# Kernel optimization log

Hardware: AMD Instinct MI355X
Metric: run time of the kernel (lower is better)

Reference implementation:

```python
import math
import jax, jax.numpy as jnp
import numpy as np

DRAGON_ITERATIONS = 12
DRAGON_SMOOTHING = 0.1


def _dragon_patterns(iterations=DRAGON_ITERATIONS, smoothing=DRAGON_SMOOTHING):
    """Deterministic (non-learned) Dragon curve patterns, matching torch impl."""
    patterns = [np.array([0.5], dtype=np.float32)]
    kernel = np.ones(3, dtype=np.float32) / 3.0
    for _ in range(1, iterations):
        prev = patterns[-1]
        n = len(prev)
        newp = np.zeros(2 * n + 1, dtype=np.float32)
        newp[:n] = prev
        newp[n] = 0.5
        newp[n + 1:] = 1.0 - prev[::-1]
        if smoothing > 0:
            # conv1d with kernel_size=3, padding=1 (zero pad) == np.convolve 'same'
            newp = np.convolve(newp, kernel, mode='same').astype(np.float32)
        newp = (newp - newp.min()) / (newp.max() - newp.min() + 1e-8)
        patterns.append(newp.astype(np.float32))
    return patterns

_PATTERNS = _dragon_patterns()


def _interp_pattern(seq_len):
    """Linearly interpolate selected dragon pattern to seq_len (static shapes)."""
    it = min(int(math.log2(seq_len)), DRAGON_ITERATIONS - 1)
    pattern = _PATTERNS[it]
    if len(pattern) == seq_len:
        w = pattern.copy()
    else:
        x_old = np.linspace(0.0, 1.0, len(pattern), dtype=np.float64)
        x_new = np.linspace(0.0, 1.0, seq_len, dtype=np.float64)
        w = np.interp(x_new, x_old, pattern.astype(np.float64)).astype(np.float32)
    return it, jnp.asarray(w)


def setup_inputs() -> dict:
    key = jax.random.key(0)
    ks = jax.random.split(key, 8)
    B, S, D = 8, 2048, 512
    query = jax.random.normal(ks[0], (B, S, D), dtype=jnp.float32)
    k = jax.random.normal(ks[1], (B, S, D), dtype=jnp.float32)
    value = jax.random.normal(ks[2], (B, S, D), dtype=jnp.float32)
    pattern_scale = jnp.ones((DRAGON_ITERATIONS,), dtype=jnp.float32)
    pattern_bias = jnp.zeros((DRAGON_ITERATIONS,), dtype=jnp.float32)
    w1 = jax.random.normal(ks[3], (DRAGON_ITERATIONS, 64), dtype=jnp.float32) * (1.0 / math.sqrt(DRAGON_ITERATIONS))
    b1 = jnp.zeros((64,), dtype=jnp.float32)
    w2 = jax.random.normal(ks[4], (64, 1), dtype=jnp.float32) * (1.0 / 8.0)
    b2 = jnp.zeros((1,), dtype=jnp.float32)
    return {"query": query, "key": k, "value": value,
            "pattern_scale": pattern_scale, "pattern_bias": pattern_bias,
            "w1": w1, "b1": b1, "w2": w2, "b2": b2}


def reference(query, key, value, pattern_scale, pattern_bias, w1, b1, w2, b2):
    B, S, D = key.shape
    it, base_w = _interp_pattern(S)
    # learned affine + softplus on dragon weights
    dragon_w = jax.nn.softplus(base_w * pattern_scale[it] + pattern_bias[it])  # [S]
    weighted_keys = key * dragon_w[None, :, None]                              # [B,S,D]
    scores = jnp.einsum('bqd,bkd->bqk', query, weighted_keys) / math.sqrt(D)   # [B,S,S]
    attn = jax.nn.softmax(scores, axis=-1)
    # blend factor from one-hot iteration features through tiny MLP
    feat = jax.nn.one_hot(it, DRAGON_ITERATIONS, dtype=query.dtype)            # [12]
    h = jax.nn.relu(feat @ w1 + b1)
    blend = jax.nn.sigmoid(h @ w2 + b2)                                        # [1]
    blend = blend[0]
    final_attn = blend * attn + (1.0 - blend) / S                              # uniform blend
    out = jnp.einsum('bqk,bkd->bqd', final_attn, value)                        # [B,S,D]
    # original does output.squeeze(1); S>1 so it's a no-op here
    return out
```

## Files before the change

### kernel.cpp

```cpp
#include <hip/hip_runtime.h>
#include <cstdint>

#define DEV __device__ __forceinline__

typedef float f32x4 __attribute__((ext_vector_type(4)));
typedef short s16x8 __attribute__((ext_vector_type(8)));

DEV unsigned short f2bf(float f){
    unsigned u = __builtin_bit_cast(unsigned, f);
    u = u + 0x7fffu + ((u >> 16) & 1u);
    return (unsigned short)(u >> 16);
}
DEV float bf2f(unsigned short h){
    unsigned u = ((unsigned)h) << 16;
    return __builtin_bit_cast(float, u);
}

typedef const void __attribute__((address_space(1)))* gcp;
typedef void __attribute__((address_space(3)))* lp;
DEV void gload_lds16(const void* g, void* l){
    __builtin_amdgcn_global_load_lds((gcp)g, (lp)l, 16, 0, 0);
}

__global__ __launch_bounds__(256) void k_stage1(
    const float* __restrict__ Q, const float* __restrict__ V,
    const float* __restrict__ scale, const float* __restrict__ bias,
    const float* __restrict__ w1, const float* __restrict__ b1,
    const float* __restrict__ w2, const float* __restrict__ b2,
    float* __restrict__ dragon_w, float* __restrict__ blend_out,
    unsigned short* __restrict__ Qb, unsigned short* __restrict__ Vt,
    float* __restrict__ vmean_part)
{
    __shared__ float sh[8704];
    int tid = threadIdx.x;
    int bx  = blockIdx.x;

    if (bx == 0){
        float* A    = sh;
        float* Bb   = sh + 4096;
        float* sred = sh + 8192;
        if (tid == 0) A[0] = 0.5f;
        __syncthreads();
        int len = 1;
        for (int it = 1; it < 12; ++it){
            int n = len, nl = 2*n + 1;
            for (int i = tid; i < nl; i += 256){
                float v;
                if (i < n)       v = A[i];
                else if (i == n) v = 0.5f;
                else             v = 1.0f - A[2*n - i];
                Bb[i] = v;
            }
            __syncthreads();
            const float third = 1.0f/3.0f;
            for (int i = tid; i < nl; i += 256){
                float s = Bb[i]*third;
                if (i > 0)    s += Bb[i-1]*third;
                if (i < nl-1) s += Bb[i+1]*third;
                A[i] = s;
            }
            __syncthreads();
            float mn = 3.4e38f, mx = -3.4e38f;
            for (int i = tid; i < nl; i += 256){ float v = A[i]; mn = fminf(mn,v); mx = fmaxf(mx,v); }
            sred[tid] = mn; sred[256 + tid] = mx;
            __syncthreads();
            for (int off = 128; off > 0; off >>= 1){
                if (tid < off){
                    sred[tid]       = fminf(sred[tid],       sred[tid+off]);
                    sred[256 + tid] = fmaxf(sred[256 + tid], sred[256 + tid + off]);
                }
                __syncthreads();
            }
            float lo = sred[0], den = sred[256] - lo + 1e-8f;
            for (int i = tid; i < nl; i += 256) A[i] = (A[i] - lo) / den;
            len = nl;
            __syncthreads();
        }
        float sc = scale[11], bi = bias[11];
        for (int i = tid; i < 2048; i += 256){
            float x = A[2*i]*sc + bi;
            dragon_w[i] = fmaxf(x, 0.f) + log1pf(__expf(-fabsf(x)));
        }
        if (tid < 64){
            float h = fmaxf(w1[11*64 + tid] + b1[tid], 0.f);
            float c = h * w2[tid];
            for (int off = 32; off > 0; off >>= 1) c += __shfl_xor(c, off, 64);
            if (tid == 0) blend_out[0] = 1.f/(1.f + __expf(-(c + b2[0])));
        }
        return;
    }

    if (bx <= 2048){
        const long long total4 = (long long)8*2048*512/4;
        long long stride = 2048LL*256;
        for (long long i = (long long)(bx-1)*256 + tid; i < total4; i += stride){
            long long base = i*4;
            const float4 q = *(const float4*)(Q + base);
            ushort4 qo;
            qo.x = f2bf(q.x); qo.y = f2bf(q.y); qo.z = f2bf(q.z); qo.w = f2bf(q.w);
            *(ushort4*)(Qb + base) = qo;
        }
        return;
    }

    int t = bx - 2049;
    int stile = t & 31, dtile = (t >> 5) & 7, b = t >> 8;
    int s0 = stile*64, d0 = dtile*64;
    float (*tile)[66] = (float(*)[66])sh;
    float* red = sh + 4352;
    int tx = tid & 63, ty = tid >> 6;
    const float* src = V + ((long long)b*2048 + s0)*512 + d0;
    #pragma unroll
    for (int r = 0; r < 16; ++r){
        int row = r*4 + ty;
        tile[row][tx] = src[(long long)row*512 + tx];
    }
    __syncthreads();
    unsigned short* dst = Vt + ((long long)b*512 + d0)*2048 + s0;
    #pragma unroll
    for (int r = 0; r < 16; ++r){
        int drow = r*4 + ty;
        dst[(long long)drow*2048 + tx] = f2bf(tile[tx][drow]);
    }
    int dcol = tid & 63, sp = tid >> 6;
    float s = 0.f;
    #pragma unroll
    for (int ii = 0; ii < 16; ++ii) s += tile[sp*16 + ii][dcol];
    red[sp*64 + dcol] = s;
    __syncthreads();
    if (sp == 0){
        float tot = red[dcol] + red[64+dcol] + red[128+dcol] + red[192+dcol];
        vmean_part[stile*4096 + b*512 + d0 + dcol] = tot * (1.0f/2048.0f);
    }
}

__global__ __launch_bounds__(256) void k_stage2(
    const float* __restrict__ K, const float* __restrict__ dragon_w,
    const float* __restrict__ vmean_part,
    unsigned short* __restrict__ Kb, float* __restrict__ vmean)
{
    int bx = blockIdx.x, tid = threadIdx.x;
    if (bx < 16){
        int idx = bx*256 + tid;
        float s = 0.f;
        #pragma unroll
        for (int st = 0; st < 32; ++st) s += vmean_part[st*4096 + idx];
        vmean[idx] = s;
        return;
    }
    const long long total4 = (long long)8*2048*512/4;
    long long stride = 2048LL*256;
    for (long long i = (long long)(bx-16)*256 + tid; i < total4; i += stride){
        long long base = i*4;
        int s = (int)((base >> 9) & 2047);
        float w = dragon_w[s];
        const float4 k = *(const float4*)(K + base);
        ushort4 ko;
        ko.x = f2bf(k.x*w); ko.y = f2bf(k.y*w); ko.z = f2bf(k.z*w); ko.w = f2bf(k.w*w);
        *(ushort4*)(Kb + base) = ko;
    }
}

#define SCALE_QK 0.04419417382415922f

__global__ __launch_bounds__(256) void k_gemm_qk(
    const unsigned short* __restrict__ Qb, const unsigned short* __restrict__ Kb,
    unsigned short* __restrict__ Sp)
{
    __shared__ unsigned short At[128*64];
    __shared__ unsigned short Bt[128*64];
    int tid = threadIdx.x;
    int lane = tid & 63, wave = tid >> 6;
    int wm = wave >> 1, wn = wave & 1;
    int ln = lane & 15, q4 = lane >> 4;
    int sx = ln & 7;
    int q0 = blockIdx.y*128, k0 = blockIdx.x*128, b = blockIdx.z;
    const unsigned short* Abase = Qb + ((long long)b*2048 + q0)*512;
    const unsigned short* Bbase = Kb + ((long long)b*2048 + k0)*512;

    f32x4 acc[4][4];
    #pragma unroll
    for (int i = 0; i < 4; ++i)
        #pragma unroll
        for (int j = 0; j < 4; ++j) acc[i][j] = (f32x4)0.0f;

    int cc = lane & 7;
    int rg = lane >> 3;
    for (int kt = 0; kt < 8; ++kt){
        #pragma unroll
        for (int c = 0; c < 4; ++c){
            int chunk = wave*4 + c;
            int row = chunk*8 + rg;
            int gc  = cc ^ (row & 7);
            gload_lds16(Abase + (long long)row*512 + kt*64 + gc*8, &At[chunk*512]);
            gload_lds16(Bbase + (long long)row*512 + kt*64 + gc*8, &Bt[chunk*512]);
        }
        __syncthreads();
        #pragma unroll
        for (int ks = 0; ks < 2; ++ks){
            s16x8 af[4], bfr[4];
            int cs = ((ks*4 + q4) ^ sx) * 8;
            #pragma unroll
            for (int i = 0; i < 4; ++i)
                af[i] = *(const s16x8*)&At[(wm*64 + i*16 + ln)*64 + cs];
            #pragma unroll
            for (int j = 0; j < 4; ++j)
                bfr[j] = *(const s16x8*)&Bt[(wn*64 + j*16 + ln)*64 + cs];
            #pragma unroll
            for (int i = 0; i < 4; ++i)
                #pragma unroll
                for (int j = 0; j < 4; ++j)
                    acc[i][j] = __builtin_amdgcn_mfma_f32_16x16x32_bf16(af[i], bfr[j], acc[i][j], 0, 0, 0);
        }
        __syncthreads();
    }
    unsigned short* outp = Sp + (long long)b*2048*2048;
    #pragma unroll
    for (int i = 0; i < 4; ++i){
        #pragma unroll
        for (int j = 0; j < 4; ++j){
            #pragma unroll
            for (int r = 0; r < 4; ++r){
                int q = q0 + wm*64 + i*16 + q4*4 + r;
                int k = k0 + wn*64 + j*16 + ln;
                float v = __expf(acc[i][j][r] * SCALE_QK);
                outp[(long long)q*2048 + k] = f2bf(v);
            }
        }
    }
}

__global__ __launch_bounds__(256) void k_gemm_pv(
    const unsigned short* __restrict__ Sp, const unsigned short* __restrict__ Vt,
    const float* __restrict__ vmean, const float* __restrict__ blendp,
    float* __restrict__ out)
{
    __shared__ unsigned short At[128*64];
    __shared__ unsigned short Bt[128*64];
    __shared__ float l_sh[128];
    int tid = threadIdx.x;
    int lane = tid & 63, wave = tid >> 6;
    int wm = wave >> 1, wn = wave & 1;
    int ln = lane & 15, q4 = lane >> 4;
    int sx = ln & 7;
    int q0 = blockIdx.y*128, d0 = blockIdx.x*128, b = blockIdx.z;
    const unsigned short* Abase = Sp + (long long)b*2048*2048 + (long long)q0*2048;
    const unsigned short* Bbase = Vt + ((long long)b*512 + d0)*2048;

    f32x4 acc[4][4];
    #pragma unroll
    for (int i = 0; i < 4; ++i)
        #pragma unroll
        for (int j = 0; j < 4; ++j) acc[i][j] = (f32x4)0.0f;
    float lsum[4] = {0.f, 0.f, 0.f, 0.f};

    int cc = lane & 7;
    int rg = lane >> 3;
    for (int kt = 0; kt < 32; ++kt){
        #pragma unroll
        for (int c = 0; c < 4; ++c){
            int chunk = wave*4 + c;
            int row = chunk*8 + rg;
            int gc  = cc ^ (row & 7);
            gload_lds16(Abase + (long long)row*2048 + kt*64 + gc*8, &At[chunk*512]);
            gload_lds16(Bbase + (long long)row*2048 + kt*64 + gc*8, &Bt[chunk*512]);
        }
        __syncthreads();
        #pragma unroll
        for (int ks = 0; ks < 2; ++ks){
            s16x8 af[4], bfr[4];
            int cs = ((ks*4 + q4) ^ sx) * 8;
            #pragma unroll
            for (int i = 0; i < 4; ++i)
                af[i] = *(const s16x8*)&At[(wm*64 + i*16 + ln)*64 + cs];
            #pragma unroll
            for (int j = 0; j < 4; ++j)
                bfr[j] = *(const s16x8*)&Bt[(wn*64 + j*16 + ln)*64 + cs];
            if (wn == 0){
                #pragma unroll
                for (int i = 0; i < 4; ++i){
                    float s = 0.f;
                    #pragma unroll
                    for (int jj = 0; jj < 8; ++jj) s += bf2f((unsigned short)af[i][jj]);
                    lsum[i] += s;
                }
            }
            #pragma unroll
            for (int i = 0; i < 4; ++i)
                #pragma unroll
                for (int j = 0; j < 4; ++j)
                    acc[i][j] = __builtin_amdgcn_mfma_f32_16x16x32_bf16(af[i], bfr[j], acc[i][j], 0, 0, 0);
        }
        __syncthreads();
    }
    if (wn == 0){
        #pragma unroll
        for (int i = 0; i < 4; ++i){
            float v = lsum[i];
            v += __shfl_xor(v, 16, 64);
            v += __shfl_xor(v, 32, 64);
            if (lane < 16) l_sh[wm*64 + i*16 + lane] = v;
        }
    }
    __syncthreads();

    float blend = blendp[0];
    float ib = 1.0f - blend;
    float* obase = out + ((long long)b*2048 + q0)*512 + d0;
    float vm[4];
    #pragma unroll
    for (int j = 0; j < 4; ++j) vm[j] = vmean[b*512 + d0 + wn*64 + j*16 + ln];
    #pragma unroll
    for (int i = 0; i < 4; ++i){
        #pragma unroll
        for (int r = 0; r < 4; ++r){
            int ql = wm*64 + i*16 + q4*4 + r;
            float linv = 1.0f / l_sh[ql];
            #pragma unroll
            for (int j = 0; j < 4; ++j){
                int dl = wn*64 + j*16 + ln;
                obase[(long long)ql*512 + dl] = blend*acc[i][j][r]*linv + ib*vm[j];
            }
        }
    }
}

extern "C" void kernel_launch(void* const* d_in, const int* in_sizes, int n_in,
                              void* d_out, int out_size, void* d_ws, size_t ws_size,
                              hipStream_t stream)
{
    (void)in_sizes; (void)n_in; (void)out_size; (void)ws_size;
    const float* Q  = (const float*)d_in[0];
    const float* K  = (const float*)d_in[1];
    const float* V  = (const float*)d_in[2];
    const float* ps = (const float*)d_in[3];
    const float* pb = (const float*)d_in[4];
    const float* w1 = (const float*)d_in[5];
    const float* b1 = (const float*)d_in[6];
    const float* w2 = (const float*)d_in[7];
    const float* b2 = (const float*)d_in[8];
    float* out = (float*)d_out;

    char* ws = (char*)d_ws;
    float* dragon_w        = (float*)(ws);
    float* blend           = (float*)(ws + 8192);
    float* vmean           = (float*)(ws + 16384);
    float* vmean_part      = (float*)(ws + 32768);
    size_t off = 32768 + (size_t)512*1024;
    unsigned short* Qb     = (unsigned short*)(ws + off);
    unsigned short* Kb     = (unsigned short*)(ws + off + (size_t)16*1024*1024);
    unsigned short* Vt     = (unsigned short*)(ws + off + (size_t)32*1024*1024);
    unsigned short* Sp     = (unsigned short*)(ws + off + (size_t)48*1024*1024);

    hipLaunchKernelGGL(k_stage1,  dim3(4097),      dim3(256), 0, stream,
                       Q, V, ps, pb, w1, b1, w2, b2, dragon_w, blend, Qb, Vt, vmean_part);
    hipLaunchKernelGGL(k_stage2,  dim3(2064),      dim3(256), 0, stream,
                       K, dragon_w, vmean_part, Kb, vmean);
    hipLaunchKernelGGL(k_gemm_qk, dim3(16, 16, 8), dim3(256), 0, stream,
                       Qb, Kb, Sp);
    hipLaunchKernelGGL(k_gemm_pv, dim3(4, 16, 8),  dim3(256), 0, stream,
                       Sp, Vt, vmean, blend, out);
}
```

Baseline: 253.2 us.

## Rewrite QK and PV GEMMs with 256-row tiles, multi-stage LDS pipelining, fused row sums

Both GEMM kernels move to 512-thread blocks with 256-row tiles and a four-slot LDS ring. Global-to-LDS loads for the next k-steps are interleaved with MFMA phases using explicit barriers, vmcnt waits and setprio. The softmax row sums are now computed in the QK epilogue from the rounded bf16 exp values and written as per-block partials, which the PV kernel reduces. This removes the per-iteration sum work from the PV inner loop. In exchange, the hand-written barrier and waitcnt scheduling is fragile, and the larger tiles reduce the grid size and may raise register pressure.

```diff
diff --git a/kernel.cpp b/kernel.cpp
--- a/kernel.cpp
+++ b/kernel.cpp
@@ -21,6 +21,11 @@
 DEV void gload_lds16(const void* g, void* l){
     __builtin_amdgcn_global_load_lds((gcp)g, (lp)l, 16, 0, 0);
 }
+
+DEV void bar(){ asm volatile("s_barrier" ::: "memory"); }
+DEV void lgkm0(){ asm volatile("s_waitcnt lgkmcnt(0)" ::: "memory"); }
+#define WAIT_VM(n) asm volatile("s_waitcnt vmcnt(" #n ")" ::: "memory")
+#define MFMA16(a,b,c) __builtin_amdgcn_mfma_f32_16x16x32_bf16(a,b,c,0,0,0)
 
 __global__ __launch_bounds__(256) void k_stage1(
     const float* __restrict__ Q, const float* __restrict__ V,
@@ -163,163 +168,276 @@
 
 #define SCALE_QK 0.04419417382415922f
 
-__global__ __launch_bounds__(256) void k_gemm_qk(
+__global__ __launch_bounds__(512, 2) void k_gemm_qk(
     const unsigned short* __restrict__ Qb, const unsigned short* __restrict__ Kb,
-    unsigned short* __restrict__ Sp)
+    unsigned short* __restrict__ Sp, float* __restrict__ lpart)
 {
-    __shared__ unsigned short At[128*64];
-    __shared__ unsigned short Bt[128*64];
-    int tid = threadIdx.x;
-    int lane = tid & 63, wave = tid >> 6;
-    int wm = wave >> 1, wn = wave & 1;
-    int ln = lane & 15, q4 = lane >> 4;
-    int sx = ln & 7;
-    int q0 = blockIdx.y*128, k0 = blockIdx.x*128, b = blockIdx.z;
-    const unsigned short* Abase = Qb + ((long long)b*2048 + q0)*512;
-    const unsigned short* Bbase = Kb + ((long long)b*2048 + k0)*512;
+    __shared__ unsigned short At[4*8192];
+    __shared__ unsigned short Bt[4*8192];
+    const int tid  = threadIdx.x;
+    const int lane = tid & 63, wave = tid >> 6;
+    const int wm = wave >> 2, wn = wave & 3;
+    const int ln = lane & 15, q4 = lane >> 4;
+    const int q0 = blockIdx.y*256, k0 = blockIdx.x*256, b = blockIdx.z;
+    const unsigned short* Ab = Qb + ((long long)b*2048 + q0)*512;
+    const unsigned short* Bb = Kb + ((long long)b*2048 + k0)*512;
+    const int cc = lane & 7, rg = lane >> 3;
+    const int gcx = cc ^ rg;
+    const int ch0 = wave*2, ch1 = wave*2 + 1;
+
+    f32x4 acc[8][4];
+    #pragma unroll
+    for (int m = 0; m < 8; ++m)
+        #pragma unroll
+        for (int n = 0; n < 4; ++n) acc[m][n] = (f32x4)0.f;
+
+    s16x8 af[8], b0[4], b1[4];
+
+    auto STA = [&](int kt, int h){
+        unsigned short* d = &At[(((kt<<1) + h) & 3) * 8192];
+        const unsigned short* s = Ab + (long long)(h*128)*512 + kt*64 + gcx*8;
+        gload_lds16(s + (long long)(ch0*8 + rg)*512, d + ch0*512);
+        gload_lds16(s + (long long)(ch1*8 + rg)*512, d + ch1*512);
+    };
+    auto STB = [&](int kt, int h){
+        unsigned short* d = &Bt[(((kt<<1) + h) & 3) * 8192];
+        const unsigned short* s = Bb + (long long)(h*128)*512 + kt*64 + gcx*8;
+        gload_lds16(s + (long long)(ch0*8 + rg)*512, d + ch0*512);
+        gload_lds16(s + (long long)(ch1*8 + rg)*512, d + ch1*512);
+    };
+    auto LDA = [&](int t, int ks){
+        const unsigned short* base = &At[(((t<<1) + wm) & 3) * 8192];
+        const int ccs = ((ks*4 + q4) ^ (ln & 7)) * 8;
+        #pragma unroll
+        for (int m = 0; m < 8; ++m)
+            af[m] = *(const s16x8*)&base[(m*16 + ln)*64 + ccs];
+    };
+    auto LDB = [&](int t, int ks, s16x8* bv){
+        const unsigned short* base = &Bt[(((t<<1) + (wn>>1)) & 3) * 8192];
+        const int ccs = ((ks*4 + q4) ^ (ln & 7)) * 8;
+        #pragma unroll
+        for (int n = 0; n < 4; ++n)
+            bv[n] = *(const s16x8*)&base[((wn&1)*64 + n*16 + ln)*64 + ccs];
+    };
+
+    STB(0,0); STB(0,1); STA(0,0); STA(0,1); STB(1,0); STB(1,1);
+    WAIT_VM(4);
+    bar();
+
+    for (int t = 0; t < 8; ++t){
+        const int t1 = (t+1) & 7, t2 = (t+2) & 7;
+        LDA(t, 0); LDB(t, 0, b0);
+        STA(t1, 0);
+        bar(); lgkm0();
+        __builtin_amdgcn_s_setprio(1);
+        #pragma unroll
+        for (int m = 0; m < 8; ++m){
+            acc[m][0] = MFMA16(af[m], b0[0], acc[m][0]);
+            acc[m][1] = MFMA16(af[m], b0[1], acc[m][1]);
+        }
+        __builtin_amdgcn_s_setprio(0);
+        bar();
+        LDB(t, 1, b1);
+        STA(t1, 1);
+        bar(); lgkm0();
+        __builtin_amdgcn_s_setprio(1);
+        #pragma unroll
+        for (int m = 0; m < 8; ++m){
+            acc[m][2] = MFMA16(af[m], b0[2], acc[m][2]);
+            acc[m][3] = MFMA16(af[m], b0[3], acc[m][3]);
+        }
+        __builtin_amdgcn_s_setprio(0);
+        bar();
+        LDA(t, 1);
+        STB(t2, 0);
+        bar(); lgkm0();
+        __builtin_amdgcn_s_setprio(1);
+        #pragma unroll
+        for (int m = 0; m < 8; ++m){
+            acc[m][0] = MFMA16(af[m], b1[0], acc[m][0]);
+            acc[m][1] = MFMA16(af[m], b1[1], acc[m][1]);
+        }
+        __builtin_amdgcn_s_setprio(0);
+        bar();
+        STB(t2, 1);
+        WAIT_VM(4);
+        bar();
+        __builtin_amdgcn_s_setprio(1);
+        #pragma unroll
+        for (int m = 0; m < 8; ++m){
+            acc[m][2] = MFMA16(af[m], b1[2], acc[m][2]);
+            acc[m][3] = MFMA16(af[m], b1[3], acc[m][3]);
+        }
+        __builtin_amdgcn_s_setprio(0);
+        bar();
+    }
+    WAIT_VM(0);
+    bar();
+
+    float* lred = (float*)At;
+    unsigned short* outp = Sp + (long long)b*2048*2048 + (long long)q0*2048 + k0;
+    #pragma unroll
+    for (int m = 0; m < 8; ++m){
+        float rs[4] = {0.f, 0.f, 0.f, 0.f};
+        #pragma unroll
+        for (int r = 0; r < 4; ++r){
+            int qrow = wm*128 + m*16 + q4*4 + r;
+            #pragma unroll
+            for (int n = 0; n < 4; ++n){
+                int kcol = wn*64 + n*16 + ln;
+                float v = __expf(acc[m][n][r] * SCALE_QK);
+                unsigned short h = f2bf(v);
+                outp[(long long)qrow*2048 + kcol] = h;
+                rs[r] += bf2f(h);
+            }
+        }
+        #pragma unroll
+        for (int r = 0; r < 4; ++r){
+            float v = rs[r];
+            v += __shfl_xor(v, 1, 16);
+            v += __shfl_xor(v, 2, 16);
+            v += __shfl_xor(v, 4, 16);
+            v += __shfl_xor(v, 8, 16);
+            if (ln == 0) lred[(wm*128 + m*16 + q4*4 + r)*4 + wn] = v;
+        }
+    }
+    bar();
+    if (tid < 256){
+        float lpv = lred[tid*4+0] + lred[tid*4+1] + lred[tid*4+2] + lred[tid*4+3];
+        lpart[((long long)b*8 + blockIdx.x)*2048 + q0 + tid] = lpv;
+    }
+}
+
+__global__ __launch_bounds__(512, 2) void k_gemm_pv(
+    const unsigned short* __restrict__ Sp, const unsigned short* __restrict__ Vt,
+    const float* __restrict__ lpart, const float* __restrict__ vmean,
+    const float* __restrict__ blendp, float* __restrict__ out)
+{
+    __shared__ unsigned short At[4*8192];
+    __shared__ unsigned short Bt[4*4096];
+    const int tid  = threadIdx.x;
+    const int lane = tid & 63, wave = tid >> 6;
+    const int wm = wave & 3, wn = wave >> 2;
+    const int ln = lane & 15, q4 = lane >> 4;
+    const int q0 = blockIdx.y*256, d0 = blockIdx.x*128, b = blockIdx.z;
+    const unsigned short* Ab = Sp + (long long)b*2048*2048 + (long long)q0*2048;
+    const unsigned short* Bb = Vt + ((long long)b*512 + d0)*2048;
+    const int cc = lane & 7, rg = lane >> 3;
+    const int gcx = cc ^ rg;
+    const int ch0 = wave*2, ch1 = wave*2 + 1;
 
     f32x4 acc[4][4];
     #pragma unroll
-    for (int i = 0; i < 4; ++i)
-        #pragma unroll
-        for (int j = 0; j < 4; ++j) acc[i][j] = (f32x4)0.0f;
-
-    int cc = lane & 7;
-    int rg = lane >> 3;
-    for (int kt = 0; kt < 8; ++kt){
-        #pragma unroll
-        for (int c = 0; c < 4; ++c){
-            int chunk = wave*4 + c;
-            int row = chunk*8 + rg;
-            int gc  = cc ^ (row & 7);
-            gload_lds16(Abase + (long long)row*512 + kt*64 + gc*8, &At[chunk*512]);
-            gload_lds16(Bbase + (long long)row*512 + kt*64 + gc*8, &Bt[chunk*512]);
-        }
-        __syncthreads();
-        #pragma unroll
-        for (int ks = 0; ks < 2; ++ks){
-            s16x8 af[4], bfr[4];
-            int cs = ((ks*4 + q4) ^ sx) * 8;
-            #pragma unroll
-            for (int i = 0; i < 4; ++i)
-                af[i] = *(const s16x8*)&At[(wm*64 + i*16 + ln)*64 + cs];
-            #pragma unroll
-            for (int j = 0; j < 4; ++j)
-                bfr[j] = *(const s16x8*)&Bt[(wn*64 + j*16 + ln)*64 + cs];
-            #pragma unroll
-            for (int i = 0; i < 4; ++i)
-                #pragma unroll
-                for (int j = 0; j < 4; ++j)
-                    acc[i][j] = __builtin_amdgcn_mfma_f32_16x16x32_bf16(af[i], bfr[j], acc[i][j], 0, 0, 0);
-        }
-        __syncthreads();
-    }
-    unsigned short* outp = Sp + (long long)b*2048*2048;
-    #pragma unroll
-    for (int i = 0; i < 4; ++i){
-        #pragma unroll
-        for (int j = 0; j < 4; ++j){
-            #pragma unroll
-            for (int r = 0; r < 4; ++r){
-                int q = q0 + wm*64 + i*16 + q4*4 + r;
-                int k = k0 + wn*64 + j*16 + ln;
-                float v = __expf(acc[i][j][r] * SCALE_QK);
-                outp[(long long)q*2048 + k] = f2bf(v);
-            }
-        }
-    }
-}
-
-__global__ __launch_bounds__(256) void k_gemm_pv(
-    const unsigned short* __restrict__ Sp, const unsigned short* __restrict__ Vt,
-    const float* __restrict__ vmean, const float* __restrict__ blendp,
-    float* __restrict__ out)
-{
-    __shared__ unsigned short At[128*64];
-    __shared__ unsigned short Bt[128*64];
-    __shared__ float l_sh[128];
-    int tid = threadIdx.x;
-    int lane = tid & 63, wave = tid >> 6;
-    int wm = wave >> 1, wn = wave & 1;
-    int ln = lane & 15, q4 = lane >> 4;
-    int sx = ln & 7;
-    int q0 = blockIdx.y*128, d0 = blockIdx.x*128, b = blockIdx.z;
-    const unsigned short* Abase = Sp + (long long)b*2048*2048 + (long long)q0*2048;
-    const unsigned short* Bbase = Vt + ((long long)b*512 + d0)*2048;
-
-    f32x4 acc[4][4];
-    #pragma unroll
-    for (int i = 0; i < 4; ++i)
-        #pragma unroll
-        for (int j = 0; j < 4; ++j) acc[i][j] = (f32x4)0.0f;
-    float lsum[4] = {0.f, 0.f, 0.f, 0.f};
-
-    int cc = lane & 7;
-    int rg = lane >> 3;
-    for (int kt = 0; kt < 32; ++kt){
-        #pragma unroll
-        for (int c = 0; c < 4; ++c){
-            int chunk = wave*4 + c;
-            int row = chunk*8 + rg;
-            int gc  = cc ^ (row & 7);
-            gload_lds16(Abase + (long long)row*2048 + kt*64 + gc*8, &At[chunk*512]);
-            gload_lds16(Bbase + (long long)row*2048 + kt*64 + gc*8, &Bt[chunk*512]);
-        }
-        __syncthreads();
-        #pragma unroll
-        for (int ks = 0; ks < 2; ++ks){
-            s16x8 af[4], bfr[4];
-            int cs = ((ks*4 + q4) ^ sx) * 8;
-            #pragma unroll
-            for (int i = 0; i < 4; ++i)
-                af[i] = *(const s16x8*)&At[(wm*64 + i*16 + ln)*64 + cs];
-            #pragma unroll
-            for (int j = 0; j < 4; ++j)
-                bfr[j] = *(const s16x8*)&Bt[(wn*64 + j*16 + ln)*64 + cs];
-            if (wn == 0){
-                #pragma unroll
-                for (int i = 0; i < 4; ++i){
-                    float s = 0.f;
-                    #pragma unroll
-                    for (int jj = 0; jj < 8; ++jj) s += bf2f((unsigned short)af[i][jj]);
-                    lsum[i] += s;
-                }
-            }
-            #pragma unroll
-            for (int i = 0; i < 4; ++i)
-                #pragma unroll
-                for (int j = 0; j < 4; ++j)
-                    acc[i][j] = __builtin_amdgcn_mfma_f32_16x16x32_bf16(af[i], bfr[j], acc[i][j], 0, 0, 0);
-        }
-        __syncthreads();
-    }
-    if (wn == 0){
-        #pragma unroll
-        for (int i = 0; i < 4; ++i){
-            float v = lsum[i];
-            v += __shfl_xor(v, 16, 64);
-            v += __shfl_xor(v, 32, 64);
-            if (lane < 16) l_sh[wm*64 + i*16 + lane] = v;
-        }
-    }
-    __syncthreads();
+    for (int m = 0; m < 4; ++m)
+        #pragma unroll
+        for (int n = 0; n < 4; ++n) acc[m][n] = (f32x4)0.f;
+
+    s16x8 af[4], b0[4], b1[4];
+
+    auto STA = [&](int kt, int h){
+        unsigned short* d = &At[(((kt<<1) + h) & 3) * 8192];
+        const unsigned short* s = Ab + (long long)(h*128)*2048 + kt*64 + gcx*8;
+        gload_lds16(s + (long long)(ch0*8 + rg)*2048, d + ch0*512);
+        gload_lds16(s + (long long)(ch1*8 + rg)*2048, d + ch1*512);
+    };
+    auto STB = [&](int kt, int h){
+        unsigned short* d = &Bt[(((kt<<1) + h) & 3) * 4096];
+        const unsigned short* s = Bb + (long long)(h*64 + wave*8 + rg)*2048 + kt*64 + gcx*8;
+        gload_lds16(s, d + wave*512);
+    };
+    auto LDA = [&](int t, int ks){
+        const unsigned short* base = &At[(((t<<1) + (wm>>1)) & 3) * 8192];
+        const int ccs = ((ks*4 + q4) ^ (ln & 7)) * 8;
+        #pragma unroll
+        for (int m = 0; m < 4; ++m)
+            af[m] = *(const s16x8*)&base[((wm&1)*64 + m*16 + ln)*64 + ccs];
+    };
+    auto LDB = [&](int t, int ks, s16x8* bv){
+        const unsigned short* base = &Bt[(((t<<1) + wn) & 3) * 4096];
+        const int ccs = ((ks*4 + q4) ^ (ln & 7)) * 8;
+        #pragma unroll
+        for (int n = 0; n < 4; ++n)
+            bv[n] = *(const s16x8*)&base[(n*16 + ln)*64 + ccs];
+    };
+
+    STB(0,0); STB(0,1); STA(0,0); STA(0,1); STB(1,0); STB(1,1);
+    WAIT_VM(2);
+    bar();
+
+    for (int t = 0; t < 32; ++t){
+        const int t1 = (t+1) & 31, t2 = (t+2) & 31;
+        LDA(t, 0); LDB(t, 0, b0);
+        STA(t1, 0);
+        bar(); lgkm0();
+        __builtin_amdgcn_s_setprio(1);
+        #pragma unroll
+        for (int m = 0; m < 4; ++m){
+            acc[m][0] = MFMA16(af[m], b0[0], acc[m][0]);
+            acc[m][1] = MFMA16(af[m], b0[1], acc[m][1]);
+        }
+        __builtin_amdgcn_s_setprio(0);
+        bar();
+        STA(t1, 1);
+        bar();
+        __builtin_amdgcn_s_setprio(1);
+        #pragma unroll
+        for (int m = 0; m < 4; ++m){
+            acc[m][2] = MFMA16(af[m], b0[2], acc[m][2]);
+            acc[m][3] = MFMA16(af[m], b0[3], acc[m][3]);
+        }
+        __builtin_amdgcn_s_setprio(0);
+        bar();
+        LDA(t, 1); LDB(t, 1, b1);
+        bar(); lgkm0();
+        __builtin_amdgcn_s_setprio(1);
+        #pragma unroll
+        for (int m = 0; m < 4; ++m){
+            acc[m][0] = MFMA16(af[m], b1[0], acc[m][0]);
+            acc[m][1] = MFMA16(af[m], b1[1], acc[m][1]);
+        }
+        __builtin_amdgcn_s_setprio(0);
+        bar();
+        STB(t2, 0); STB(t2, 1);
+        WAIT_VM(2);
+        bar();
+        __builtin_amdgcn_s_setprio(1);
+        #pragma unroll
+        for (int m = 0; m < 4; ++m){
+            acc[m][2] = MFMA16(af[m], b1[2], acc[m][2]);
+            acc[m][3] = MFMA16(af[m], b1[3], acc[m][3]);
+        }
+        __builtin_amdgcn_s_setprio(0);
+        bar();
+    }
+    WAIT_VM(0);
+    bar();
+
+    float* l_sh = (float*)Bt;
+    if (tid < 256){
+        float s = 0.f;
+        #pragma unroll
+        for (int kb = 0; kb < 8; ++kb)
+            s += lpart[((long long)b*8 + kb)*2048 + q0 + tid];
+        l_sh[tid] = 1.0f / s;
+    }
+    bar();
 
     float blend = blendp[0];
     float ib = 1.0f - blend;
     float* obase = out + ((long long)b*2048 + q0)*512 + d0;
     float vm[4];
     #pragma unroll
-    for (int j = 0; j < 4; ++j) vm[j] = vmean[b*512 + d0 + wn*64 + j*16 + ln];
-    #pragma unroll
-    for (int i = 0; i < 4; ++i){
+    for (int n = 0; n < 4; ++n) vm[n] = vmean[b*512 + d0 + wn*64 + n*16 + ln];
+    #pragma unroll
+    for (int m = 0; m < 4; ++m){
         #pragma unroll
         for (int r = 0; r < 4; ++r){
-            int ql = wm*64 + i*16 + q4*4 + r;
-            float linv = 1.0f / l_sh[ql];
+            int ql = wm*64 + m*16 + q4*4 + r;
+            float linv = l_sh[ql];
             #pragma unroll
-            for (int j = 0; j < 4; ++j){
-                int dl = wn*64 + j*16 + ln;
-                obase[(long long)ql*512 + dl] = blend*acc[i][j][r]*linv + ib*vm[j];
+            for (int n = 0; n < 4; ++n){
+                int dl = wn*64 + n*16 + ln;
+                obase[(long long)ql*512 + dl] = blend*acc[m][n][r]*linv + ib*vm[n];
             }
         }
     }
@@ -351,13 +469,14 @@
     unsigned short* Kb     = (unsigned short*)(ws + off + (size_t)16*1024*1024);
     unsigned short* Vt     = (unsigned short*)(ws + off + (size_t)32*1024*1024);
     unsigned short* Sp     = (unsigned short*)(ws + off + (size_t)48*1024*1024);
-
-    hipLaunchKernelGGL(k_stage1,  dim3(4097),      dim3(256), 0, stream,
+    float* lpart           = vmean_part;
+
+    hipLaunchKernelGGL(k_stage1,  dim3(4097),     dim3(256), 0, stream,
                        Q, V, ps, pb, w1, b1, w2, b2, dragon_w, blend, Qb, Vt, vmean_part);
-    hipLaunchKernelGGL(k_stage2,  dim3(2064),      dim3(256), 0, stream,
+    hipLaunchKernelGGL(k_stage2,  dim3(2064),     dim3(256), 0, stream,
                        K, dragon_w, vmean_part, Kb, vmean);
-    hipLaunchKernelGGL(k_gemm_qk, dim3(16, 16, 8), dim3(256), 0, stream,
-                       Qb, Kb, Sp);
-    hipLaunchKernelGGL(k_gemm_pv, dim3(4, 16, 8),  dim3(256), 0, stream,
-                       Sp, Vt, vmean, blend, out);
-}
+    hipLaunchKernelGGL(k_gemm_qk, dim3(8, 8, 8),  dim3(512), 0, stream,
+                       Qb, Kb, Sp, lpart);
+    hipLaunchKernelGGL(k_gemm_pv, dim3(4, 8, 8),  dim3(512), 0, stream,
+                       Sp, Vt, lpart, vmean, blend, out);
+}
```

Result: slower. 260.4 us (+2.9%).

## Move softmax row-sum into QK epilogue, remap blocks per XCD, vectorize V transpose

Applied to the files above, without the earlier changes.

The QK GEMM epilogue now sums the rounded exp values per row and writes per-key-tile partial sums, which the PV kernel reduces instead of summing the A fragments inside its main loop. Both GEMMs switch to a 1D grid whose block indices are remapped so consecutive blocks on the same XCD share a batch and neighbouring tiles, to improve L2 reuse. The V transpose in stage1 uses float4 loads and ushort4 stores with a padded tile of stride 67. This adds a small partial-sum buffer plus an extra shuffle and reduction in the QK epilogue.

```diff
diff --git a/kernel.cpp b/kernel.cpp
--- a/kernel.cpp
+++ b/kernel.cpp
@@ -106,21 +106,28 @@
     int t = bx - 2049;
     int stile = t & 31, dtile = (t >> 5) & 7, b = t >> 8;
     int s0 = stile*64, d0 = dtile*64;
-    float (*tile)[66] = (float(*)[66])sh;
-    float* red = sh + 4352;
-    int tx = tid & 63, ty = tid >> 6;
+    float (*tile)[67] = (float(*)[67])sh;
+    float* red = sh + 4288;
+    int c4 = tid & 15, rr = tid >> 4;
     const float* src = V + ((long long)b*2048 + s0)*512 + d0;
     #pragma unroll
-    for (int r = 0; r < 16; ++r){
-        int row = r*4 + ty;
-        tile[row][tx] = src[(long long)row*512 + tx];
+    for (int p = 0; p < 4; ++p){
+        int row = p*16 + rr;
+        const float4 v = *(const float4*)(src + (long long)row*512 + c4*4);
+        tile[row][c4*4+0] = v.x; tile[row][c4*4+1] = v.y;
+        tile[row][c4*4+2] = v.z; tile[row][c4*4+3] = v.w;
     }
     __syncthreads();
     unsigned short* dst = Vt + ((long long)b*512 + d0)*2048 + s0;
     #pragma unroll
-    for (int r = 0; r < 16; ++r){
-        int drow = r*4 + ty;
-        dst[(long long)drow*2048 + tx] = f2bf(tile[tx][drow]);
+    for (int p = 0; p < 4; ++p){
+        int d = p*16 + rr;
+        ushort4 o;
+        o.x = f2bf(tile[c4*4+0][d]);
+        o.y = f2bf(tile[c4*4+1][d]);
+        o.z = f2bf(tile[c4*4+2][d]);
+        o.w = f2bf(tile[c4*4+3][d]);
+        *(ushort4*)(dst + (long long)d*2048 + c4*4) = o;
     }
     int dcol = tid & 63, sp = tid >> 6;
     float s = 0.f;
@@ -165,7 +172,7 @@
 
 __global__ __launch_bounds__(256) void k_gemm_qk(
     const unsigned short* __restrict__ Qb, const unsigned short* __restrict__ Kb,
-    unsigned short* __restrict__ Sp)
+    unsigned short* __restrict__ Sp, float* __restrict__ lpart)
 {
     __shared__ unsigned short At[128*64];
     __shared__ unsigned short Bt[128*64];
@@ -174,7 +181,9 @@
     int wm = wave >> 1, wn = wave & 1;
     int ln = lane & 15, q4 = lane >> 4;
     int sx = ln & 7;
-    int q0 = blockIdx.y*128, k0 = blockIdx.x*128, b = blockIdx.z;
+    int lid = (blockIdx.x & 7)*256 + (blockIdx.x >> 3);
+    int kb = lid & 15, qb = (lid >> 4) & 15, b = lid >> 8;
+    int q0 = qb*128, k0 = kb*128;
     const unsigned short* Abase = Qb + ((long long)b*2048 + q0)*512;
     const unsigned short* Bbase = Kb + ((long long)b*2048 + k0)*512;
 
@@ -214,9 +223,11 @@
         }
         __syncthreads();
     }
+    float* lred = (float*)At;
     unsigned short* outp = Sp + (long long)b*2048*2048;
     #pragma unroll
     for (int i = 0; i < 4; ++i){
+        float rs[4] = {0.f, 0.f, 0.f, 0.f};
         #pragma unroll
         for (int j = 0; j < 4; ++j){
             #pragma unroll
@@ -224,26 +235,41 @@
                 int q = q0 + wm*64 + i*16 + q4*4 + r;
                 int k = k0 + wn*64 + j*16 + ln;
                 float v = __expf(acc[i][j][r] * SCALE_QK);
-                outp[(long long)q*2048 + k] = f2bf(v);
-            }
-        }
-    }
+                unsigned short h = f2bf(v);
+                outp[(long long)q*2048 + k] = h;
+                rs[r] += bf2f(h);
+            }
+        }
+        #pragma unroll
+        for (int r = 0; r < 4; ++r){
+            float v = rs[r];
+            v += __shfl_xor(v, 1, 16);
+            v += __shfl_xor(v, 2, 16);
+            v += __shfl_xor(v, 4, 16);
+            v += __shfl_xor(v, 8, 16);
+            if (ln == 0) lred[(wm*64 + i*16 + q4*4 + r)*2 + wn] = v;
+        }
+    }
+    __syncthreads();
+    if (tid < 128)
+        lpart[((long long)b*16 + kb)*2048 + q0 + tid] = lred[tid*2] + lred[tid*2+1];
 }
 
 __global__ __launch_bounds__(256) void k_gemm_pv(
     const unsigned short* __restrict__ Sp, const unsigned short* __restrict__ Vt,
-    const float* __restrict__ vmean, const float* __restrict__ blendp,
-    float* __restrict__ out)
+    const float* __restrict__ lpart, const float* __restrict__ vmean,
+    const float* __restrict__ blendp, float* __restrict__ out)
 {
     __shared__ unsigned short At[128*64];
     __shared__ unsigned short Bt[128*64];
-    __shared__ float l_sh[128];
     int tid = threadIdx.x;
     int lane = tid & 63, wave = tid >> 6;
     int wm = wave >> 1, wn = wave & 1;
     int ln = lane & 15, q4 = lane >> 4;
     int sx = ln & 7;
-    int q0 = blockIdx.y*128, d0 = blockIdx.x*128, b = blockIdx.z;
+    int lid = (blockIdx.x & 7)*64 + (blockIdx.x >> 3);
+    int db = lid & 3, qb = (lid >> 2) & 15, b = lid >> 6;
+    int q0 = qb*128, d0 = db*128;
     const unsigned short* Abase = Sp + (long long)b*2048*2048 + (long long)q0*2048;
     const unsigned short* Bbase = Vt + ((long long)b*512 + d0)*2048;
 
@@ -252,7 +278,6 @@
     for (int i = 0; i < 4; ++i)
         #pragma unroll
         for (int j = 0; j < 4; ++j) acc[i][j] = (f32x4)0.0f;
-    float lsum[4] = {0.f, 0.f, 0.f, 0.f};
 
     int cc = lane & 7;
     int rg = lane >> 3;
@@ -276,15 +301,6 @@
             #pragma unroll
             for (int j = 0; j < 4; ++j)
                 bfr[j] = *(const s16x8*)&Bt[(wn*64 + j*16 + ln)*64 + cs];
-            if (wn == 0){
-                #pragma unroll
-                for (int i = 0; i < 4; ++i){
-                    float s = 0.f;
-                    #pragma unroll
-                    for (int jj = 0; jj < 8; ++jj) s += bf2f((unsigned short)af[i][jj]);
-                    lsum[i] += s;
-                }
-            }
             #pragma unroll
             for (int i = 0; i < 4; ++i)
                 #pragma unroll
@@ -293,14 +309,14 @@
         }
         __syncthreads();
     }
-    if (wn == 0){
-        #pragma unroll
-        for (int i = 0; i < 4; ++i){
-            float v = lsum[i];
-            v += __shfl_xor(v, 16, 64);
-            v += __shfl_xor(v, 32, 64);
-            if (lane < 16) l_sh[wm*64 + i*16 + lane] = v;
-        }
+
+    float* l_sh = (float*)Bt;
+    if (tid < 128){
+        float s = 0.f;
+        #pragma unroll
+        for (int kb = 0; kb < 16; ++kb)
+            s += lpart[((long long)b*16 + kb)*2048 + q0 + tid];
+        l_sh[tid] = 1.0f / s;
     }
     __syncthreads();
 
@@ -315,7 +331,7 @@
         #pragma unroll
         for (int r = 0; r < 4; ++r){
             int ql = wm*64 + i*16 + q4*4 + r;
-            float linv = 1.0f / l_sh[ql];
+            float linv = l_sh[ql];
             #pragma unroll
             for (int j = 0; j < 4; ++j){
                 int dl = wn*64 + j*16 + ln;
@@ -351,13 +367,14 @@
     unsigned short* Kb     = (unsigned short*)(ws + off + (size_t)16*1024*1024);
     unsigned short* Vt     = (unsigned short*)(ws + off + (size_t)32*1024*1024);
     unsigned short* Sp     = (unsigned short*)(ws + off + (size_t)48*1024*1024);
-
-    hipLaunchKernelGGL(k_stage1,  dim3(4097),      dim3(256), 0, stream,
+    float* lpart           = (float*)(ws + off + (size_t)112*1024*1024);
+
+    hipLaunchKernelGGL(k_stage1,  dim3(4097), dim3(256), 0, stream,
                        Q, V, ps, pb, w1, b1, w2, b2, dragon_w, blend, Qb, Vt, vmean_part);
-    hipLaunchKernelGGL(k_stage2,  dim3(2064),      dim3(256), 0, stream,
+    hipLaunchKernelGGL(k_stage2,  dim3(2064), dim3(256), 0, stream,
                        K, dragon_w, vmean_part, Kb, vmean);
-    hipLaunchKernelGGL(k_gemm_qk, dim3(16, 16, 8), dim3(256), 0, stream,
-                       Qb, Kb, Sp);
-    hipLaunchKernelGGL(k_gemm_pv, dim3(4, 16, 8),  dim3(256), 0, stream,
-                       Sp, Vt, vmean, blend, out);
-}
+    hipLaunchKernelGGL(k_gemm_qk, dim3(2048), dim3(256), 0, stream,
+                       Qb, Kb, Sp, lpart);
+    hipLaunchKernelGGL(k_gemm_pv, dim3(512),  dim3(256), 0, stream,
+                       Sp, Vt, lpart, vmean, blend, out);
+}
```

Measured after the change: 255.9 us. Within noise of the previous version (+1.1%).
